# Kernel tuning notes

Measured on AMD Instinct MI355X. Metric: run time of the kernel, lower is better.

The kernel has to match this reference:

```python
import jax, jax.numpy as jnp
import numpy as np

B, T, E, H = 1, 4096, 768, 12
DH = E // H


def setup_inputs() -> dict:
    key = jax.random.key(0)
    ks = jax.random.split(key, 10)
    s = 0.02
    inp = {
        "queries": jax.random.normal(ks[0], (B, T, E), jnp.float32),
        "values": jax.random.normal(ks[1], (B, T, E), jnp.float32),
        # causal mask (1 = keep, 0 = masked), matches masked_fill(mask == 0, -1e9)
        "mask": jnp.tril(jnp.ones((T, T), jnp.int32))[None, None, :, :],
        "Wq": jax.random.normal(ks[2], (E, E), jnp.float32) * s,
        "bq": jnp.zeros((E,), jnp.float32),
        "Wk": jax.random.normal(ks[3], (E, E), jnp.float32) * s,
        "bk": jnp.zeros((E,), jnp.float32),
        "Wv": jax.random.normal(ks[4], (E, E), jnp.float32) * s,
        "bv": jnp.zeros((E,), jnp.float32),
        "Wo": jax.random.normal(ks[5], (E, E), jnp.float32) * s,
        "bo": jnp.zeros((E,), jnp.float32),
    }
    return inp


def _split_heads(x):
    # [B,T,E] -> [B,H,T,DH]
    return x.reshape(B, T, H, DH).transpose(0, 2, 1, 3)


def reference(queries, values, mask, Wq, bq, Wk, bk, Wv, bv, Wo, bo):
    # torch nn.Linear: y = x @ W.T + b
    q = _split_heads(queries @ Wq.T + bq)
    k = _split_heads(values @ Wk.T + bk)
    v = _split_heads(values @ Wv.T + bv)
    scale = 1.0 / np.sqrt(DH).astype(np.float32)
    logits = jnp.einsum("bhqd,bhkd->bhqk", q, k) * scale  # [B,H,T,T]
    logits = jnp.where(mask == 0, jnp.float32(-1e9), logits)
    probs = jax.nn.softmax(logits, axis=-1)
    ctx = jnp.einsum("bhqk,bhkd->bhqd", probs, v)  # [B,H,T,DH]
    ctx = ctx.transpose(0, 2, 1, 3).reshape(B, T, E)
    return ctx @ Wo.T + bo
```

## Files before the change

### kernel.cpp

```cpp
#include <hip/hip_runtime.h>
#include <hip/hip_bf16.h>


typedef __hip_bfloat16 bf16;
typedef __attribute__((ext_vector_type(8))) short short8;
typedef __attribute__((ext_vector_type(4))) short short4v;
typedef __attribute__((ext_vector_type(4))) float f32x4;

#define TSEQ 4096
#define NHEAD 12
#define DHEAD 64
#define EMB 768

#if defined(__HIP_DEVICE_COMPILE__)
#define MFMA16(a, b, c) __builtin_amdgcn_mfma_f32_16x16x16bf16_1k(a, b, c, 0, 0, 0)
#else
#define MFMA16(a, b, c) (c)
#endif

typedef const __attribute__((address_space(1))) unsigned int* gptr_t;
typedef __attribute__((address_space(3))) unsigned int* lptr_t;

__device__ __forceinline__ void load_lds16(const void* g, void* l) {
    __builtin_amdgcn_global_load_lds((gptr_t)g, (lptr_t)l, 16, 0, 0);
}

__device__ __forceinline__ float b2f(short s) {
    unsigned u = ((unsigned)(unsigned short)s) << 16;
    float f;
    __builtin_memcpy(&f, &u, 4);
    return f;
}

__device__ __forceinline__ short f2bs(float f) {
    bf16 h = __float2bfloat16(f);
    short s;
    __builtin_memcpy(&s, &h, 2);
    return s;
}

struct CvtJob { const float* src; bf16* dst; int n; };
struct CvtArgs { CvtJob j[6]; };

__global__ __launch_bounds__(256) void cvt_kernel(CvtArgs a) {
    const CvtJob jb = a.j[blockIdx.y];
    const int i = (blockIdx.x * 256 + threadIdx.x) * 8;
    if (i >= jb.n) return;
    const float4 x0 = *(const float4*)(jb.src + i);
    const float4 x1 = *(const float4*)(jb.src + i + 4);
    bf16 tmp[8];
    tmp[0] = __float2bfloat16(x0.x); tmp[1] = __float2bfloat16(x0.y);
    tmp[2] = __float2bfloat16(x0.z); tmp[3] = __float2bfloat16(x0.w);
    tmp[4] = __float2bfloat16(x1.x); tmp[5] = __float2bfloat16(x1.y);
    tmp[6] = __float2bfloat16(x1.z); tmp[7] = __float2bfloat16(x1.w);
    *(short8*)(jb.dst + i) = *(const short8*)tmp;
}

template<int NF>
__device__ __forceinline__ void gemm_t(
    const bf16* __restrict__ A, const bf16* __restrict__ W,
    const float* __restrict__ bias,
    bf16* __restrict__ outb, float* __restrict__ outf,
    const int mode, const float scale, const int m0, const int n0,
    bf16* sA, bf16* sB)
{
    const int tid  = threadIdx.x;
    const int lane = tid & 63;
    const int wave = tid >> 6;
    const int wr = wave >> 1, wc = wave & 1;
    const int lg = lane >> 4, lr = lane & 15;

    f32x4 acc[4][NF];
#pragma unroll
    for (int m = 0; m < 4; ++m)
#pragma unroll
        for (int n = 0; n < NF; ++n)
            acc[m][n] = (f32x4){0.f, 0.f, 0.f, 0.f};

    for (int k0 = 0; k0 < EMB; k0 += 64) {
        if (k0) __syncthreads();
#pragma unroll
        for (int is = 0; is < 4; ++is) {
            const int chunk = is * 256 + tid;
            const int row = chunk >> 3;
            const int csw = (chunk & 7) ^ (row & 7);
            load_lds16(A + (size_t)(m0 + row) * EMB + k0 + csw * 8,
                       sA + is * 2048 + wave * 512);
        }
#pragma unroll
        for (int is = 0; is < NF; ++is) {
            const int chunk = is * 256 + tid;
            const int row = chunk >> 3;
            const int csw = (chunk & 7) ^ (row & 7);
            load_lds16(W + (size_t)(n0 + row) * EMB + k0 + csw * 8,
                       sB + is * 2048 + wave * 512);
        }
        __syncthreads();

        short8 af[4][2], bfv[NF][2];
#pragma unroll
        for (int m = 0; m < 4; ++m)
#pragma unroll
            for (int kk = 0; kk < 2; ++kk) {
                const int row = wr * 64 + m * 16 + lr;
                const int cc = (kk * 4 + lg) ^ (row & 7);
                af[m][kk] = *(const short8*)(sA + row * 64 + cc * 8);
            }
#pragma unroll
        for (int n = 0; n < NF; ++n)
#pragma unroll
            for (int kk = 0; kk < 2; ++kk) {
                const int row = wc * (NF * 16) + n * 16 + lr;
                const int cc = (kk * 4 + lg) ^ (row & 7);
                bfv[n][kk] = *(const short8*)(sB + row * 64 + cc * 8);
            }
#pragma unroll
        for (int kk = 0; kk < 2; ++kk)
#pragma unroll
            for (int m = 0; m < 4; ++m)
#pragma unroll
                for (int n = 0; n < NF; ++n)
                    acc[m][n] = __builtin_amdgcn_mfma_f32_16x16x32_bf16(
                        af[m][kk], bfv[n][kk], acc[m][n], 0, 0, 0);
    }

#pragma unroll
    for (int n = 0; n < NF; ++n) {
        const int o = n0 + wc * (NF * 16) + n * 16 + lr;
        const float bv = bias[o];
#pragma unroll
        for (int m = 0; m < 4; ++m) {
            const int tbase = m0 + wr * 64 + m * 16 + lg * 4;
#pragma unroll
            for (int r = 0; r < 4; ++r) {
                const float v = (acc[m][n][r] + bv) * scale;
                const int t = tbase + r;
                if (mode == 0)
                    outb[(size_t)(o >> 6) * TSEQ * DHEAD + (size_t)t * DHEAD + (o & 63)] =
                        __float2bfloat16(v);
                else if (mode == 1)
                    outb[(size_t)(o >> 6) * DHEAD * TSEQ + (size_t)(o & 63) * TSEQ + t] =
                        __float2bfloat16(v);
                else
                    outf[(size_t)t * EMB + o] = v;
            }
        }
    }
}

struct QkvArgs {
    const bf16 *xq, *xv, *Wq, *Wk, *Wv;
    const float *bq, *bk, *bv;
    bf16 *qo, *ko, *vto;
};

__global__ __launch_bounds__(256) void qkv_gemm(QkvArgs a) {
    __shared__ __attribute__((aligned(16))) bf16 sA[128 * 64];
    __shared__ __attribute__((aligned(16))) bf16 sB[128 * 64];
    const int z = blockIdx.z;
    const bf16* A = (z == 0) ? a.xq : a.xv;
    const bf16* W = (z == 0) ? a.Wq : (z == 1 ? a.Wk : a.Wv);
    const float* b = (z == 0) ? a.bq : (z == 1 ? a.bk : a.bv);
    bf16* o = (z == 0) ? a.qo : (z == 1 ? a.ko : a.vto);
    const int mode = (z == 2) ? 1 : 0;
    const float scale = (z == 0) ? 0.18033688011112042f : 1.0f;
    gemm_t<4>(A, W, b, o, nullptr, mode, scale, blockIdx.x * 128, blockIdx.y * 128, sA, sB);
}

__global__ __launch_bounds__(256) void out_gemm(
    const bf16* __restrict__ ctx, const bf16* __restrict__ Wo,
    const float* __restrict__ bo, float* __restrict__ out)
{
    __shared__ __attribute__((aligned(16))) bf16 sA[128 * 64];
    __shared__ __attribute__((aligned(16))) bf16 sB[64 * 64];
    gemm_t<2>(ctx, Wo, bo, nullptr, out, 2, 1.0f, blockIdx.x * 128, blockIdx.y * 64, sA, sB);
}

struct AttnState {
    f32x4 O[4];
    float m, l;
};

__device__ __forceinline__ void stage_tile(
    const bf16* __restrict__ Kh, const bf16* __restrict__ Vh,
    bf16* sK, bf16* sV, const int kv0, const int tid)
{
    const int wave = tid >> 6;
#pragma unroll
    for (int is = 0; is < 2; ++is) {
        const int chunk = is * 256 + tid;
        const int row = chunk >> 3;
        const int csw = (chunk & 7) ^ (row & 7);
        load_lds16(Kh + (size_t)(kv0 + row) * DHEAD + csw * 8,
                   sK + is * 2048 + wave * 512);
        load_lds16(Vh + (size_t)row * TSEQ + kv0 + csw * 8,
                   sV + is * 2048 + wave * 512);
    }
}

__device__ __forceinline__ void attn_tile(
    const bf16* sK, const bf16* sV,
    const short8 (&qf)[2], AttnState& st,
    const int kv0, const int qw, const int lane)
{
    const int lg = lane >> 4, lr = lane & 15;
    if (kv0 > qw + 15) return;

    f32x4 s[4];
#pragma unroll
    for (int n = 0; n < 4; ++n) s[n] = (f32x4){0.f, 0.f, 0.f, 0.f};
    short8 kf[4][2];
#pragma unroll
    for (int n = 0; n < 4; ++n)
#pragma unroll
        for (int kk = 0; kk < 2; ++kk) {
            const int row = n * 16 + lr;
            const int cc = (kk * 4 + lg) ^ (row & 7);
            kf[n][kk] = *(const short8*)(sK + row * 64 + cc * 8);
        }
#pragma unroll
    for (int kk = 0; kk < 2; ++kk)
#pragma unroll
        for (int n = 0; n < 4; ++n)
            s[n] = __builtin_amdgcn_mfma_f32_16x16x32_bf16(
                kf[n][kk], qf[kk], s[n], 0, 0, 0);

    if (kv0 + 63 > qw) {
        const int qi = qw + lr;
#pragma unroll
        for (int n = 0; n < 4; ++n) {
            const int kb = kv0 + n * 16 + lg * 4;
#pragma unroll
            for (int r = 0; r < 4; ++r)
                if (kb + r > qi) s[n][r] = -3.0e38f;
        }
    }

    float mx = s[0][0];
#pragma unroll
    for (int n = 0; n < 4; ++n)
#pragma unroll
        for (int r = 0; r < 4; ++r) mx = fmaxf(mx, s[n][r]);
    mx = fmaxf(mx, __shfl_xor(mx, 16));
    mx = fmaxf(mx, __shfl_xor(mx, 32));

    const float mn = fmaxf(st.m, mx);
    const float al = __builtin_amdgcn_exp2f(st.m - mn);
    st.m = mn;

    float rs = 0.f;
    short4v pq[4];
#pragma unroll
    for (int n = 0; n < 4; ++n) {
#pragma unroll
        for (int r = 0; r < 4; ++r) {
            const float p = __builtin_amdgcn_exp2f(s[n][r] - mn);
            s[n][r] = p;
            rs += p;
        }
        pq[n][0] = f2bs(s[n][0]); pq[n][1] = f2bs(s[n][1]);
        pq[n][2] = f2bs(s[n][2]); pq[n][3] = f2bs(s[n][3]);
    }
    rs += __shfl_xor(rs, 16);
    rs += __shfl_xor(rs, 32);
    st.l = st.l * al + rs;

#pragma unroll
    for (int nd = 0; nd < 4; ++nd)
#pragma unroll
        for (int r = 0; r < 4; ++r)
            st.O[nd][r] *= al;

#pragma unroll
    for (int nd = 0; nd < 4; ++nd) {
        const int row = nd * 16 + lr;
        f32x4 o = st.O[nd];
#pragma unroll
        for (int n = 0; n < 4; ++n) {
            const int c16 = (n * 2 + (lg >> 1)) ^ (row & 7);
            const short4v va = *(const short4v*)(sV + row * 64 + c16 * 8 + (lg & 1) * 4);
            o = MFMA16(va, pq[n], o);
        }
        st.O[nd] = o;
    }
}

__global__ __launch_bounds__(256, 4) void attn_kernel(
    const bf16* __restrict__ Q, const bf16* __restrict__ K,
    const bf16* __restrict__ VT, bf16* __restrict__ Opart,
    float* __restrict__ ml, const int nch_max)
{
    __shared__ __attribute__((aligned(16))) bf16 sK0[64 * 64];
    __shared__ __attribute__((aligned(16))) bf16 sK1[64 * 64];
    __shared__ __attribute__((aligned(16))) bf16 sV0[64 * 64];
    __shared__ __attribute__((aligned(16))) bf16 sV1[64 * 64];

    const int tid  = threadIdx.x;
    const int lane = tid & 63;
    const int wave = tid >> 6;
    const int lg = lane >> 4, lr = lane & 15;
    const int h  = blockIdx.z;
    const int c  = blockIdx.y;
    const int bx = gridDim.x - 1 - blockIdx.x;
    const int q0 = bx * 64;
    const int qw = q0 + wave * 16;

    const int S = bx + 1;
    const int nchb = (nch_max > 1) ? min((S + 7) >> 3, nch_max) : 1;
    if (c >= nchb) return;
    const int t0 = (c * S) / nchb;
    const int t1 = ((c + 1) * S) / nchb;

    const bf16* Qh = Q  + (size_t)h * TSEQ * DHEAD;
    const bf16* Kh = K  + (size_t)h * TSEQ * DHEAD;
    const bf16* Vh = VT + (size_t)h * DHEAD * TSEQ;

    short8 qf[2];
#pragma unroll
    for (int kk = 0; kk < 2; ++kk)
        qf[kk] = *(const short8*)(Qh + (size_t)(qw + lr) * DHEAD + kk * 32 + lg * 8);

    AttnState st;
#pragma unroll
    for (int nd = 0; nd < 4; ++nd) st.O[nd] = (f32x4){0.f, 0.f, 0.f, 0.f};
    st.m = -3.0e38f; st.l = 0.f;

    stage_tile(Kh, Vh, sK0, sV0, t0 * 64, tid);
    __syncthreads();

    int it = t0;
    while (it < t1) {
        if (it + 1 < t1) stage_tile(Kh, Vh, sK1, sV1, (it + 1) * 64, tid);
        attn_tile(sK0, sV0, qf, st, it * 64, qw, lane);
        __syncthreads();
        ++it;
        if (it >= t1) break;
        if (it + 1 < t1) stage_tile(Kh, Vh, sK0, sV0, (it + 1) * 64, tid);
        attn_tile(sK1, sV1, qf, st, it * 64, qw, lane);
        __syncthreads();
        ++it;
    }

    const int u = (h * 64 + bx) * nch_max + c;
    bf16* op = Opart + (size_t)u * 4096;
    float* mlp = ml + (size_t)u * 128;
    const int q = wave * 16 + lr;
#pragma unroll
    for (int nd = 0; nd < 4; ++nd) {
        short4v ov;
        ov[0] = f2bs(st.O[nd][0]); ov[1] = f2bs(st.O[nd][1]);
        ov[2] = f2bs(st.O[nd][2]); ov[3] = f2bs(st.O[nd][3]);
        *(short4v*)(op + q * 64 + nd * 16 + lg * 4) = ov;
    }
    if (lg == 0) {
        mlp[q] = st.m;
        mlp[64 + q] = st.l;
    }
}

__global__ __launch_bounds__(256) void combine_kernel(
    const bf16* __restrict__ Opart, const float* __restrict__ ml,
    bf16* __restrict__ ctx, const int nch_max)
{
    const int h  = blockIdx.y;
    const int bx = blockIdx.x;
    const int tid = threadIdx.x;
    const int row = tid >> 2;
    const int dp  = (tid & 3) * 16;
    const int ub = (h * 64 + bx) * nch_max;
    const int S = bx + 1;
    const int nchb = (nch_max > 1) ? min((S + 7) >> 3, nch_max) : 1;

    float M = -3.0e38f;
    for (int c = 0; c < nchb; ++c)
        M = fmaxf(M, ml[(size_t)(ub + c) * 128 + row]);

    float L = 0.f;
    float acc[16];
#pragma unroll
    for (int i = 0; i < 16; ++i) acc[i] = 0.f;
    for (int c = 0; c < nchb; ++c) {
        const float mc = ml[(size_t)(ub + c) * 128 + row];
        const float lc = ml[(size_t)(ub + c) * 128 + 64 + row];
        const float w = __builtin_amdgcn_exp2f(mc - M);
        L += lc * w;
        const bf16* op = Opart + ((size_t)(ub + c) * 64 + row) * 64 + dp;
        const short8 v0 = *(const short8*)op;
        const short8 v1 = *(const short8*)(op + 8);
#pragma unroll
        for (int i = 0; i < 8; ++i) acc[i] += w * b2f(v0[i]);
#pragma unroll
        for (int i = 0; i < 8; ++i) acc[8 + i] += w * b2f(v1[i]);
    }
    const float invL = 1.0f / L;

    bf16 outv[16];
#pragma unroll
    for (int i = 0; i < 16; ++i) outv[i] = __float2bfloat16(acc[i] * invL);
    const int t = bx * 64 + row;
    bf16* dst = ctx + (size_t)t * EMB + h * DHEAD + dp;
    *(short8*)dst = *(const short8*)outv;
    *(short8*)(dst + 8) = *(const short8*)(outv + 8);
}

extern "C" void kernel_launch(void* const* d_in, const int* in_sizes, int n_in,
                              void* d_out, int out_size, void* d_ws, size_t ws_size,
                              hipStream_t stream) {
    const float* queries = (const float*)d_in[0];
    const float* values  = (const float*)d_in[1];
    const float* Wq = (const float*)d_in[3];
    const float* bq = (const float*)d_in[4];
    const float* Wk = (const float*)d_in[5];
    const float* bk = (const float*)d_in[6];
    const float* Wv = (const float*)d_in[7];
    const float* bv = (const float*)d_in[8];
    const float* Wo = (const float*)d_in[9];
    const float* bo = (const float*)d_in[10];
    float* out = (float*)d_out;

    const size_t NTE = (size_t)TSEQ * EMB;
    const size_t WSZ = (size_t)EMB * EMB;
    bf16* ws  = (bf16*)d_ws;
    bf16* qb  = ws;
    bf16* vb  = qb + NTE;
    bf16* wqb = vb + NTE;
    bf16* wkb = wqb + WSZ;
    bf16* wvb = wkb + WSZ;
    bf16* wob = wvb + WSZ;
    bf16* qh  = wob + WSZ;
    bf16* kh  = qh + NTE;
    bf16* vth = kh + NTE;
    bf16* ctx = qb;

    const size_t fixed_elems = 5 * NTE + 4 * WSZ;
    int nch = 8;
    for (;;) {
        const size_t units = (size_t)NHEAD * (TSEQ / 64) * nch;
        const size_t need = fixed_elems * 2 + units * 4096 * 2 + units * 128 * 4;
        if (ws_size >= need || nch == 1) break;
        nch = (nch == 8) ? 4 : 1;
    }
    const size_t units = (size_t)NHEAD * (TSEQ / 64) * nch;
    bf16* opart = ws + fixed_elems;
    float* ml = (float*)(opart + units * 4096);

    CvtArgs ca;
    ca.j[0] = {queries, qb,  (int)NTE};
    ca.j[1] = {values,  vb,  (int)NTE};
    ca.j[2] = {Wq,      wqb, (int)WSZ};
    ca.j[3] = {Wk,      wkb, (int)WSZ};
    ca.j[4] = {Wv,      wvb, (int)WSZ};
    ca.j[5] = {Wo,      wob, (int)WSZ};
    cvt_kernel<<<dim3((NTE + 2047) / 2048, 6), 256, 0, stream>>>(ca);

    QkvArgs a{qb, vb, wqb, wkb, wvb, bq, bk, bv, qh, kh, vth};
    qkv_gemm<<<dim3(TSEQ / 128, EMB / 128, 3), 256, 0, stream>>>(a);
    attn_kernel<<<dim3(TSEQ / 64, nch, NHEAD), 256, 0, stream>>>(qh, kh, vth, opart, ml, nch);
    combine_kernel<<<dim3(TSEQ / 64, NHEAD), 256, 0, stream>>>(opart, ml, ctx, nch);
    out_gemm<<<dim3(TSEQ / 128, EMB / 64), 256, 0, stream>>>(ctx, wob, bo, out);
}
```

Measured before the change: 127.2 us.

## Widen attention blocks to 128 queries with 8 waves sharing K/V tiles

The attention kernel now runs 512 threads (8 waves) covering 128 query rows per block instead of 64. Each K/V tile staged in LDS is reused by twice as many waves, and staging needs one load per thread instead of two. Split bookkeeping is adjusted so each half-block writes its own 64-row partial unit, and combine recomputes the chunk count from the paired block. The max and exp-sum reductions are also rewritten as balanced trees to shorten dependency chains. The cost is coarser causal load balancing, since the lower waves in a block idle on diagonal tiles, and fewer blocks in the grid.

Result: slower. 150.6 us (+18.4%).

```diff
diff --git a/kernel.cpp b/kernel.cpp
--- a/kernel.cpp
+++ b/kernel.cpp
@@ -186,16 +186,10 @@
     bf16* sK, bf16* sV, const int kv0, const int tid)
 {
     const int wave = tid >> 6;
-#pragma unroll
-    for (int is = 0; is < 2; ++is) {
-        const int chunk = is * 256 + tid;
-        const int row = chunk >> 3;
-        const int csw = (chunk & 7) ^ (row & 7);
-        load_lds16(Kh + (size_t)(kv0 + row) * DHEAD + csw * 8,
-                   sK + is * 2048 + wave * 512);
-        load_lds16(Vh + (size_t)row * TSEQ + kv0 + csw * 8,
-                   sV + is * 2048 + wave * 512);
-    }
+    const int row = tid >> 3;
+    const int csw = (tid & 7) ^ (row & 7);
+    load_lds16(Kh + (size_t)(kv0 + row) * DHEAD + csw * 8, sK + wave * 512);
+    load_lds16(Vh + (size_t)row * TSEQ + kv0 + csw * 8, sV + wave * 512);
 }
 
 __device__ __forceinline__ void attn_tile(
@@ -236,11 +230,11 @@
         }
     }
 
-    float mx = s[0][0];
-#pragma unroll
-    for (int n = 0; n < 4; ++n)
-#pragma unroll
-        for (int r = 0; r < 4; ++r) mx = fmaxf(mx, s[n][r]);
+    const float a0 = fmaxf(fmaxf(s[0][0], s[0][1]), fmaxf(s[0][2], s[0][3]));
+    const float a1 = fmaxf(fmaxf(s[1][0], s[1][1]), fmaxf(s[1][2], s[1][3]));
+    const float a2 = fmaxf(fmaxf(s[2][0], s[2][1]), fmaxf(s[2][2], s[2][3]));
+    const float a3 = fmaxf(fmaxf(s[3][0], s[3][1]), fmaxf(s[3][2], s[3][3]));
+    float mx = fmaxf(fmaxf(a0, a1), fmaxf(a2, a3));
     mx = fmaxf(mx, __shfl_xor(mx, 16));
     mx = fmaxf(mx, __shfl_xor(mx, 32));
 
@@ -248,19 +242,19 @@
     const float al = __builtin_amdgcn_exp2f(st.m - mn);
     st.m = mn;
 
-    float rs = 0.f;
+    float rsn[4];
     short4v pq[4];
 #pragma unroll
     for (int n = 0; n < 4; ++n) {
-#pragma unroll
-        for (int r = 0; r < 4; ++r) {
-            const float p = __builtin_amdgcn_exp2f(s[n][r] - mn);
-            s[n][r] = p;
-            rs += p;
-        }
-        pq[n][0] = f2bs(s[n][0]); pq[n][1] = f2bs(s[n][1]);
-        pq[n][2] = f2bs(s[n][2]); pq[n][3] = f2bs(s[n][3]);
-    }
+        const float p0 = __builtin_amdgcn_exp2f(s[n][0] - mn);
+        const float p1 = __builtin_amdgcn_exp2f(s[n][1] - mn);
+        const float p2 = __builtin_amdgcn_exp2f(s[n][2] - mn);
+        const float p3 = __builtin_amdgcn_exp2f(s[n][3] - mn);
+        rsn[n] = (p0 + p1) + (p2 + p3);
+        pq[n][0] = f2bs(p0); pq[n][1] = f2bs(p1);
+        pq[n][2] = f2bs(p2); pq[n][3] = f2bs(p3);
+    }
+    float rs = (rsn[0] + rsn[1]) + (rsn[2] + rsn[3]);
     rs += __shfl_xor(rs, 16);
     rs += __shfl_xor(rs, 32);
     st.l = st.l * al + rs;
@@ -285,7 +279,7 @@
     }
 }
 
-__global__ __launch_bounds__(256, 4) void attn_kernel(
+__global__ __launch_bounds__(512, 4) void attn_kernel(
     const bf16* __restrict__ Q, const bf16* __restrict__ K,
     const bf16* __restrict__ VT, bf16* __restrict__ Opart,
     float* __restrict__ ml, const int nch_max)
@@ -302,10 +296,10 @@
     const int h  = blockIdx.z;
     const int c  = blockIdx.y;
     const int bx = gridDim.x - 1 - blockIdx.x;
-    const int q0 = bx * 64;
+    const int q0 = bx * 128;
     const int qw = q0 + wave * 16;
 
-    const int S = bx + 1;
+    const int S = 2 * bx + 2;
     const int nchb = (nch_max > 1) ? min((S + 7) >> 3, nch_max) : 1;
     if (c >= nchb) return;
     const int t0 = (c * S) / nchb;
@@ -341,10 +335,10 @@
         ++it;
     }
 
-    const int u = (h * 64 + bx) * nch_max + c;
+    const int u = (h * 64 + bx * 2 + (wave >> 2)) * nch_max + c;
     bf16* op = Opart + (size_t)u * 4096;
     float* mlp = ml + (size_t)u * 128;
-    const int q = wave * 16 + lr;
+    const int q = (wave & 3) * 16 + lr;
 #pragma unroll
     for (int nd = 0; nd < 4; ++nd) {
         short4v ov;
@@ -368,7 +362,7 @@
     const int row = tid >> 2;
     const int dp  = (tid & 3) * 16;
     const int ub = (h * 64 + bx) * nch_max;
-    const int S = bx + 1;
+    const int S = 2 * (bx >> 1) + 2;
     const int nchb = (nch_max > 1) ? min((S + 7) >> 3, nch_max) : 1;
 
     float M = -3.0e38f;
@@ -455,7 +449,7 @@
 
     QkvArgs a{qb, vb, wqb, wkb, wvb, bq, bk, bv, qh, kh, vth};
     qkv_gemm<<<dim3(TSEQ / 128, EMB / 128, 3), 256, 0, stream>>>(a);
-    attn_kernel<<<dim3(TSEQ / 64, nch, NHEAD), 256, 0, stream>>>(qh, kh, vth, opart, ml, nch);
+    attn_kernel<<<dim3(TSEQ / 128, nch, NHEAD), 512, 0, stream>>>(qh, kh, vth, opart, ml, nch);
     combine_kernel<<<dim3(TSEQ / 64, NHEAD), 256, 0, stream>>>(opart, ml, ctx, nch);
     out_gemm<<<dim3(TSEQ / 128, EMB / 64), 256, 0, stream>>>(ctx, wob, bo, out);
 }
```
